# Kernel optimization log

Measured on AMD Instinct MI355X. Metric: run time of the kernel, lower is better.

Reference implementation:

```python
import jax, jax.numpy as jnp
import numpy as np

LENGTH = 200
SHIFT = 150
NFFT = 256
EPS = 1e-7  # keras backend epsilon
LN10 = float(np.log(10.0))


def _make_kernels():
    # real_kernel[n, k] = cos(2*pi*k*n/nfft); imag_kernel[n, k] = -sin(2*pi*k*n/nfft)
    # taps k >= length are zeroed in the original (kernel[length-nfft:] = 0),
    # so we build the truncated [nfft, length] kernels directly.
    n = np.arange(NFFT)[:, None]
    k = np.arange(LENGTH)[None, :]
    ang = 2.0 * np.pi * n * k / NFFT
    real = np.cos(ang).astype(np.float32)
    imag = (-np.sin(ang)).astype(np.float32)
    return jnp.asarray(real), jnp.asarray(imag)


def setup_inputs() -> dict:
    key = jax.random.key(0)
    B = 64
    S = 200 + 150 * 3199  # 480050, satisfies (S - length) % shift == 0
    x = jax.random.normal(key, (B, S, 1), dtype=jnp.float32)
    real_kernel, imag_kernel = _make_kernels()
    return {"x": x, "real_kernel": real_kernel, "imag_kernel": imag_kernel}


def reference(x, real_kernel, imag_kernel):
    B, S, C = x.shape  # C == 1
    # normalize_signal: zero mean / unit std over (time, channel)
    mu = jnp.mean(x, axis=(1, 2), keepdims=True)
    sd = jnp.std(x, axis=(1, 2), keepdims=True)
    x = (x - mu) / (sd + EPS)

    sig = x[:, :, 0]  # [B, S]
    T = (S - LENGTH) // SHIFT + 1  # frames; zero-padding to nfft is a no-op since padded taps hit zeroed kernel rows
    idx = SHIFT * jnp.arange(T)[:, None] + jnp.arange(LENGTH)[None, :]  # [T, length]
    frames = sig[:, idx]  # [B, T, length]

    # strided conv1d against dense DFT kernels == framed GEMM
    real_part = jnp.einsum("btl,nl->btn", frames, real_kernel)  # [B, T, nfft]
    imag_part = jnp.einsum("btl,nl->btn", frames, imag_kernel)

    # mode == 'log': log10 of clipped magnitude
    mag = jnp.sqrt(jnp.square(real_part) + jnp.square(imag_part))
    fft = jnp.log(jnp.maximum(mag, EPS)) / LN10

    # permute (0,2,1) -> [B, nfft, T], keep first nfft//2 bins, add channel dim
    fft = jnp.transpose(fft, (0, 2, 1))[:, : NFFT // 2, :, None]  # [B, 128, T, 1]

    # normalize_feature: zero mean / unit std over frequency axis
    fmu = jnp.mean(fft, axis=1, keepdims=True)
    fsd = jnp.std(fft, axis=1, keepdims=True)
    fft = (fft - fmu) / (fsd + EPS)
    return fft
```

## Files before the change

### kernel.cpp

```cpp
#include <hip/hip_runtime.h>
#include <math.h>
#include <stdint.h>

#define BATCH 64
#define SLEN  480050
#define TFR   3200
#define FLEN  200
#define FSH   150
#define NBINS 128
#define NCOL  256
#define NKC   7

#define WS_SUM 0
#define WS_MU  2048
#define WS_OR  2112
#define WS_OI  2240
#define WS_TABI_BYTES 16384

typedef __attribute__((ext_vector_type(8))) short bf16x8;
typedef __attribute__((ext_vector_type(4))) float f32x4;

__device__ inline unsigned pack2bf(float a, float b) {
    unsigned ua = __builtin_bit_cast(unsigned, a);
    unsigned ub = __builtin_bit_cast(unsigned, b);
    ua = (ua + 0x7FFFu + ((ua >> 16) & 1u)) >> 16;
    ub = (ub + 0x7FFFu + ((ub >> 16) & 1u)) >> 16;
    return ua | (ub << 16);
}

__device__ inline void gll16(const void* g, void* l) {
    __builtin_amdgcn_global_load_lds(
        (const __attribute__((address_space(1))) void*)g,
        (__attribute__((address_space(3))) void*)l, 16, 0, 0);
}

__global__ __launch_bounds__(256) void k_sum_partial(const float* __restrict__ x,
                                                     float* __restrict__ ws) {
    int blk = blockIdx.x;
    int b = blk >> 5, c = blk & 31;
    const float2* row = (const float2*)(x + (size_t)b * SLEN);
    const int n2 = SLEN / 2;
    const int per = (n2 + 31) / 32;
    int start = c * per;
    int end = start + per; if (end > n2) end = n2;
    float s = 0.f;
    for (int i = start + threadIdx.x; i < end; i += 256) {
        float2 v = row[i];
        s += v.x + v.y;
    }
    #pragma unroll
    for (int off = 1; off < 64; off <<= 1) s += __shfl_xor(s, off);
    __shared__ float ls[4];
    int wave = threadIdx.x >> 6, lane = threadIdx.x & 63;
    if (lane == 0) ls[wave] = s;
    __syncthreads();
    if (threadIdx.x == 0)
        ws[WS_SUM + b * 32 + c] = ls[0] + ls[1] + ls[2] + ls[3];
}

__global__ __launch_bounds__(64) void k_final(float* __restrict__ ws) {
    int b = threadIdx.x;
    if (b < BATCH) {
        float s = 0.f;
        #pragma unroll
        for (int c = 0; c < 32; ++c) s += ws[WS_SUM + b * 32 + c];
        ws[WS_MU + b] = s / (float)SLEN;
    }
}

__global__ __launch_bounds__(256) void k_colsum(const float* __restrict__ rk,
                                                const float* __restrict__ ik,
                                                float* __restrict__ ws) {
    int n = blockIdx.x;
    int l = threadIdx.x;
    float cr = 0.f, ci = 0.f;
    if (l < FLEN) {
        cr = rk[n * FLEN + l];
        ci = ik[n * FLEN + l];
    }
    #pragma unroll
    for (int off = 1; off < 64; off <<= 1) {
        cr += __shfl_xor(cr, off);
        ci += __shfl_xor(ci, off);
    }
    __shared__ float lr[4], li[4];
    int wave = threadIdx.x >> 6, lane = threadIdx.x & 63;
    if (lane == 0) { lr[wave] = cr; li[wave] = ci; }
    __syncthreads();
    if (threadIdx.x == 0) {
        ws[WS_OR + n] = lr[0] + lr[1] + lr[2] + lr[3];
        ws[WS_OI + n] = li[0] + li[1] + li[2] + li[3];
    }
}

__global__ __launch_bounds__(256) void k_tabsplit(const float* __restrict__ rk,
                                                  const float* __restrict__ ik,
                                                  float* __restrict__ ws) {
    int e = blockIdx.x * 256 + threadIdx.x;
    if (e >= NCOL * 112) return;
    int c = e / 112;
    int p = e - c * 112;
    int k = p * 2;
    int n = c & 127;
    const float* src = (c & 128) ? ik : rk;
    float v0 = (k     < FLEN) ? src[n * FLEN + k]     : 0.f;
    float v1 = (k + 1 < FLEN) ? src[n * FLEN + k + 1] : 0.f;
    unsigned hi = pack2bf(v0, v1);
    float h0 = __builtin_bit_cast(float, hi << 16);
    float h1 = __builtin_bit_cast(float, hi & 0xFFFF0000u);
    unsigned lo = pack2bf(v0 - h0, v1 - h1);
    int kc = k >> 5;
    int kb = (k & 31) * 2;
    int sb = (kb >> 4) ^ ((c >> 1) & 3);
    char* base = (char*)ws + WS_TABI_BYTES + kc * 32768 + c * 64 + (sb << 4) + (kb & 15);
    *(unsigned*)base = hi;
    *(unsigned*)(base + 16384) = lo;
}

__global__ __launch_bounds__(256, 2) void k_main(const float* __restrict__ x,
                                                 const float* __restrict__ ws,
                                                 float* __restrict__ out) {
    __shared__ __align__(16) unsigned char smem[65536];

    const int tid    = threadIdx.x;
    const int b      = blockIdx.y;
    const int t0     = blockIdx.x * 64;
    const int lane   = tid & 63;
    const int w      = tid >> 6;
    const int lanelo = lane & 15;
    const int lq     = lane >> 4;
    const int sbswz  = (lanelo >> 1) & 3;

    const float* xb  = x + (size_t)b * SLEN;
    const char* tabI = (const char*)ws + WS_TABI_BYTES;

    #pragma unroll
    for (int i = 0; i < 8; ++i)
        gll16(tabI + (w * 8 + i) * 1024 + lane * 16, smem + (w * 8 + i) * 1024);
    __syncthreads();

    f32x4 acc[16];
    #pragma unroll
    for (int nt = 0; nt < 16; ++nt) acc[nt] = (f32x4){0.f, 0.f, 0.f, 0.f};

    const float* arow = xb + (size_t)(t0 + w * 16 + lanelo) * FSH;

    for (int kc = 0; kc < NKC; ++kc) {
        if (kc < NKC - 1) {
            const char* src = tabI + (size_t)(kc + 1) * 32768;
            unsigned char* db = smem + ((kc + 1) & 1) * 32768;
            #pragma unroll
            for (int i = 0; i < 8; ++i)
                gll16(src + (w * 8 + i) * 1024 + lane * 16, db + (w * 8 + i) * 1024);
        }

        float a[8];
        if (kc < NKC - 1 || lq == 0) {
            const float2* s2 = (const float2*)(arow + kc * 32 + lq * 8);
            float2 p0 = s2[0], p1 = s2[1], p2 = s2[2], p3 = s2[3];
            a[0] = p0.x; a[1] = p0.y; a[2] = p1.x; a[3] = p1.y;
            a[4] = p2.x; a[5] = p2.y; a[6] = p3.x; a[7] = p3.y;
        } else {
            #pragma unroll
            for (int i = 0; i < 8; ++i) a[i] = 0.f;
        }
        unsigned hw[4], lw[4];
        #pragma unroll
        for (int q = 0; q < 4; ++q) {
            hw[q] = pack2bf(a[2 * q], a[2 * q + 1]);
            float h0 = __builtin_bit_cast(float, hw[q] << 16);
            float h1 = __builtin_bit_cast(float, hw[q] & 0xFFFF0000u);
            lw[q] = pack2bf(a[2 * q] - h0, a[2 * q + 1] - h1);
        }
        bf16x8 ah = __builtin_bit_cast(bf16x8, *(uint4*)hw);
        bf16x8 al = __builtin_bit_cast(bf16x8, *(uint4*)lw);

        const unsigned char* Bb = smem + (kc & 1) * 32768;
        #pragma unroll
        for (int nt = 0; nt < 16; ++nt) {
            int off = (nt * 16 + lanelo) * 64 + ((lq ^ sbswz) << 4);
            bf16x8 bh = *(const bf16x8*)(Bb + off);
            bf16x8 bl = *(const bf16x8*)(Bb + 16384 + off);
            acc[nt] = __builtin_amdgcn_mfma_f32_16x16x32_bf16(al, bh, acc[nt], 0, 0, 0);
            acc[nt] = __builtin_amdgcn_mfma_f32_16x16x32_bf16(ah, bl, acc[nt], 0, 0, 0);
            acc[nt] = __builtin_amdgcn_mfma_f32_16x16x32_bf16(ah, bh, acc[nt], 0, 0, 0);
        }
        __syncthreads();
    }

    float mu = ws[WS_MU + b];
    float v[8][4];
    #pragma unroll
    for (int nt = 0; nt < 8; ++nt) {
        float orr = ws[WS_OR + nt * 16 + lanelo];
        float oii = ws[WS_OI + nt * 16 + lanelo];
        #pragma unroll
        for (int j = 0; j < 4; ++j) {
            float re = acc[nt][j]     - mu * orr;
            float im = acc[nt + 8][j] - mu * oii;
            float s = fmaf(re, re, im * im);
            float lg = 0.5f * __log2f(s);
            v[nt][j] = fmaxf(lg, -23.2534966f);
        }
    }
    #pragma unroll
    for (int j = 0; j < 4; ++j) {
        float s = 0.f, q = 0.f;
        #pragma unroll
        for (int nt = 0; nt < 8; ++nt) {
            s += v[nt][j];
            q = fmaf(v[nt][j], v[nt][j], q);
        }
        #pragma unroll
        for (int off = 1; off < 16; off <<= 1) {
            s += __shfl_xor(s, off);
            q += __shfl_xor(q, off);
        }
        float mean = s * (1.f / 128.f);
        float var  = fmaxf(q * (1.f / 128.f) - mean * mean, 0.f);
        float sc   = 1.f / (sqrtf(var) + 3.3219281e-7f);
        #pragma unroll
        for (int nt = 0; nt < 8; ++nt) v[nt][j] = (v[nt][j] - mean) * sc;
    }

    float* Tw = (float*)(smem + w * 8192);
    #pragma unroll
    for (int nt = 0; nt < 8; ++nt) {
        int n = nt * 16 + lanelo;
        int swzl = (lq ^ (n & 3) ^ ((n >> 2) & 1)) << 2;
        *(float4*)(Tw + n * 16 + swzl) =
            make_float4(v[nt][0], v[nt][1], v[nt][2], v[nt][3]);
    }
    float* ob = out + (size_t)b * NBINS * TFR + t0 + w * 16;
    #pragma unroll
    for (int p = 0; p < 2; ++p) {
        int n = p * 64 + lane;
        int sw = (n & 3) ^ ((n >> 2) & 1);
        float4 r0 = *(float4*)(Tw + n * 16 + ((0 ^ sw) << 2));
        float4 r1 = *(float4*)(Tw + n * 16 + ((1 ^ sw) << 2));
        float4 r2 = *(float4*)(Tw + n * 16 + ((2 ^ sw) << 2));
        float4 r3 = *(float4*)(Tw + n * 16 + ((3 ^ sw) << 2));
        float4* dst = (float4*)(ob + (size_t)n * TFR);
        dst[0] = r0; dst[1] = r1; dst[2] = r2; dst[3] = r3;
    }
}

extern "C" void kernel_launch(void* const* d_in, const int* in_sizes, int n_in,
                              void* d_out, int out_size, void* d_ws, size_t ws_size,
                              hipStream_t stream) {
    const float* x  = (const float*)d_in[0];
    const float* rk = (const float*)d_in[1];
    const float* ik = (const float*)d_in[2];
    float* out = (float*)d_out;
    float* ws  = (float*)d_ws;

    k_sum_partial<<<BATCH * 32, 256, 0, stream>>>(x, ws);
    k_final<<<1, 64, 0, stream>>>(ws);
    k_colsum<<<NBINS, 256, 0, stream>>>(rk, ik, ws);
    k_tabsplit<<<112, 256, 0, stream>>>(rk, ik, ws);
    k_main<<<dim3(TFR / 64, BATCH), 256, 0, stream>>>(x, ws, out);
}
```

Measured before the change: 316.4 us.

## Merge prep kernels into one launch and double M-tile per wave in main GEMM

Folds the four preprocessing kernels into a single k_aux launch. The per-batch mean is now computed inside k_main from the partial sums, which removes launch overhead and one dependent launch. k_main now processes 128 frames per block, two 16-row M tiles per wave, so each B fragment loaded from LDS feeds six MFMAs instead of three and the table staging is amortised over twice the frames. The input split now uses the hip bf16 conversion intrinsics. Costs are twice the accumulator registers (128 floats) under a 2-blocks-per-CU bound, which risks spills, and half as many blocks (1600), which reduces parallelism.

```diff
diff --git a/kernel.cpp b/kernel.cpp
--- a/kernel.cpp
+++ b/kernel.cpp
@@ -1,4 +1,5 @@
 #include <hip/hip_runtime.h>
+#include <hip/hip_bf16.h>
 #include <math.h>
 #include <stdint.h>
 
@@ -12,7 +13,6 @@
 #define NKC   7
 
 #define WS_SUM 0
-#define WS_MU  2048
 #define WS_OR  2112
 #define WS_OI  2240
 #define WS_TABI_BYTES 16384
@@ -34,87 +34,83 @@
         (__attribute__((address_space(3))) void*)l, 16, 0, 0);
 }
 
-__global__ __launch_bounds__(256) void k_sum_partial(const float* __restrict__ x,
-                                                     float* __restrict__ ws) {
+__global__ __launch_bounds__(256) void k_aux(const float* __restrict__ x,
+                                             const float* __restrict__ rk,
+                                             const float* __restrict__ ik,
+                                             float* __restrict__ ws) {
     int blk = blockIdx.x;
-    int b = blk >> 5, c = blk & 31;
-    const float2* row = (const float2*)(x + (size_t)b * SLEN);
-    const int n2 = SLEN / 2;
-    const int per = (n2 + 31) / 32;
-    int start = c * per;
-    int end = start + per; if (end > n2) end = n2;
-    float s = 0.f;
-    for (int i = start + threadIdx.x; i < end; i += 256) {
-        float2 v = row[i];
-        s += v.x + v.y;
-    }
-    #pragma unroll
-    for (int off = 1; off < 64; off <<= 1) s += __shfl_xor(s, off);
-    __shared__ float ls[4];
-    int wave = threadIdx.x >> 6, lane = threadIdx.x & 63;
-    if (lane == 0) ls[wave] = s;
-    __syncthreads();
-    if (threadIdx.x == 0)
-        ws[WS_SUM + b * 32 + c] = ls[0] + ls[1] + ls[2] + ls[3];
-}
-
-__global__ __launch_bounds__(64) void k_final(float* __restrict__ ws) {
-    int b = threadIdx.x;
-    if (b < BATCH) {
+    if (blk < 2048) {
+        int b = blk >> 5, c = blk & 31;
+        const float2* row = (const float2*)(x + (size_t)b * SLEN);
+        const int n2 = SLEN / 2;
+        const int per = (n2 + 31) / 32;
+        int start = c * per;
+        int end = start + per; if (end > n2) end = n2;
         float s = 0.f;
-        #pragma unroll
-        for (int c = 0; c < 32; ++c) s += ws[WS_SUM + b * 32 + c];
-        ws[WS_MU + b] = s / (float)SLEN;
-    }
-}
-
-__global__ __launch_bounds__(256) void k_colsum(const float* __restrict__ rk,
-                                                const float* __restrict__ ik,
-                                                float* __restrict__ ws) {
-    int n = blockIdx.x;
-    int l = threadIdx.x;
-    float cr = 0.f, ci = 0.f;
-    if (l < FLEN) {
-        cr = rk[n * FLEN + l];
-        ci = ik[n * FLEN + l];
-    }
-    #pragma unroll
-    for (int off = 1; off < 64; off <<= 1) {
-        cr += __shfl_xor(cr, off);
-        ci += __shfl_xor(ci, off);
-    }
-    __shared__ float lr[4], li[4];
-    int wave = threadIdx.x >> 6, lane = threadIdx.x & 63;
-    if (lane == 0) { lr[wave] = cr; li[wave] = ci; }
-    __syncthreads();
-    if (threadIdx.x == 0) {
-        ws[WS_OR + n] = lr[0] + lr[1] + lr[2] + lr[3];
-        ws[WS_OI + n] = li[0] + li[1] + li[2] + li[3];
-    }
-}
-
-__global__ __launch_bounds__(256) void k_tabsplit(const float* __restrict__ rk,
-                                                  const float* __restrict__ ik,
-                                                  float* __restrict__ ws) {
-    int e = blockIdx.x * 256 + threadIdx.x;
-    if (e >= NCOL * 112) return;
-    int c = e / 112;
-    int p = e - c * 112;
-    int k = p * 2;
-    int n = c & 127;
-    const float* src = (c & 128) ? ik : rk;
-    float v0 = (k     < FLEN) ? src[n * FLEN + k]     : 0.f;
-    float v1 = (k + 1 < FLEN) ? src[n * FLEN + k + 1] : 0.f;
-    unsigned hi = pack2bf(v0, v1);
-    float h0 = __builtin_bit_cast(float, hi << 16);
-    float h1 = __builtin_bit_cast(float, hi & 0xFFFF0000u);
-    unsigned lo = pack2bf(v0 - h0, v1 - h1);
-    int kc = k >> 5;
-    int kb = (k & 31) * 2;
-    int sb = (kb >> 4) ^ ((c >> 1) & 3);
-    char* base = (char*)ws + WS_TABI_BYTES + kc * 32768 + c * 64 + (sb << 4) + (kb & 15);
-    *(unsigned*)base = hi;
-    *(unsigned*)(base + 16384) = lo;
+        for (int i = start + threadIdx.x; i < end; i += 256) {
+            float2 v = row[i];
+            s += v.x + v.y;
+        }
+        #pragma unroll
+        for (int off = 1; off < 64; off <<= 1) s += __shfl_xor(s, off);
+        __shared__ float ls[4];
+        int wave = threadIdx.x >> 6, lane = threadIdx.x & 63;
+        if (lane == 0) ls[wave] = s;
+        __syncthreads();
+        if (threadIdx.x == 0)
+            ws[WS_SUM + b * 32 + c] = ls[0] + ls[1] + ls[2] + ls[3];
+    } else if (blk < 2160) {
+        int e = (blk - 2048) * 256 + threadIdx.x;
+        int c = e / 112;
+        int p = e - c * 112;
+        int k = p * 2;
+        int n = c & 127;
+        const float* src = (c & 128) ? ik : rk;
+        float v0 = (k     < FLEN) ? src[n * FLEN + k]     : 0.f;
+        float v1 = (k + 1 < FLEN) ? src[n * FLEN + k + 1] : 0.f;
+        unsigned hi = pack2bf(v0, v1);
+        float h0 = __builtin_bit_cast(float, hi << 16);
+        float h1 = __builtin_bit_cast(float, hi & 0xFFFF0000u);
+        unsigned lo = pack2bf(v0 - h0, v1 - h1);
+        int kc = k >> 5;
+        int kb = (k & 31) * 2;
+        int sb = (kb >> 4) ^ ((c >> 1) & 3);
+        char* base = (char*)ws + WS_TABI_BYTES + kc * 32768 + c * 64 + (sb << 4) + (kb & 15);
+        *(unsigned*)base = hi;
+        *(unsigned*)(base + 16384) = lo;
+    } else {
+        int n = blk - 2160;
+        int l = threadIdx.x;
+        float cr = 0.f, ci = 0.f;
+        if (l < FLEN) {
+            cr = rk[n * FLEN + l];
+            ci = ik[n * FLEN + l];
+        }
+        #pragma unroll
+        for (int off = 1; off < 64; off <<= 1) {
+            cr += __shfl_xor(cr, off);
+            ci += __shfl_xor(ci, off);
+        }
+        __shared__ float lr[4], li[4];
+        int wave = threadIdx.x >> 6, lane = threadIdx.x & 63;
+        if (lane == 0) { lr[wave] = cr; li[wave] = ci; }
+        __syncthreads();
+        if (threadIdx.x == 0) {
+            ws[WS_OR + n] = lr[0] + lr[1] + lr[2] + lr[3];
+            ws[WS_OI + n] = li[0] + li[1] + li[2] + li[3];
+        }
+    }
+}
+
+__device__ inline void split8(const float* __restrict__ a, bf16x8& hv, bf16x8& lv) {
+    #pragma unroll
+    for (int i = 0; i < 8; ++i) {
+        __hip_bfloat16 hb = __float2bfloat16(a[i]);
+        float hf = __bfloat162float(hb);
+        __hip_bfloat16 lb = __float2bfloat16(a[i] - hf);
+        hv[i] = __builtin_bit_cast(short, hb);
+        lv[i] = __builtin_bit_cast(short, lb);
+    }
 }
 
 __global__ __launch_bounds__(256, 2) void k_main(const float* __restrict__ x,
@@ -124,7 +120,7 @@
 
     const int tid    = threadIdx.x;
     const int b      = blockIdx.y;
-    const int t0     = blockIdx.x * 64;
+    const int t0     = blockIdx.x * 128;
     const int lane   = tid & 63;
     const int w      = tid >> 6;
     const int lanelo = lane & 15;
@@ -134,16 +130,22 @@
     const float* xb  = x + (size_t)b * SLEN;
     const char* tabI = (const char*)ws + WS_TABI_BYTES;
 
+    float msum = 0.f;
+    #pragma unroll
+    for (int c = 0; c < 32; ++c) msum += ws[WS_SUM + b * 32 + c];
+    const float mu = msum * (1.0f / (float)SLEN);
+
     #pragma unroll
     for (int i = 0; i < 8; ++i)
         gll16(tabI + (w * 8 + i) * 1024 + lane * 16, smem + (w * 8 + i) * 1024);
     __syncthreads();
 
-    f32x4 acc[16];
-    #pragma unroll
-    for (int nt = 0; nt < 16; ++nt) acc[nt] = (f32x4){0.f, 0.f, 0.f, 0.f};
-
-    const float* arow = xb + (size_t)(t0 + w * 16 + lanelo) * FSH;
+    f32x4 acc[32];
+    #pragma unroll
+    for (int q = 0; q < 32; ++q) acc[q] = (f32x4){0.f, 0.f, 0.f, 0.f};
+
+    const float* arow0 = xb + (size_t)(t0 + w * 32 + lanelo) * FSH;
+    const float* arow1 = arow0 + (size_t)16 * FSH;
 
     for (int kc = 0; kc < NKC; ++kc) {
         if (kc < NKC - 1) {
@@ -154,26 +156,22 @@
                 gll16(src + (w * 8 + i) * 1024 + lane * 16, db + (w * 8 + i) * 1024);
         }
 
-        float a[8];
-        if (kc < NKC - 1 || lq == 0) {
-            const float2* s2 = (const float2*)(arow + kc * 32 + lq * 8);
-            float2 p0 = s2[0], p1 = s2[1], p2 = s2[2], p3 = s2[3];
-            a[0] = p0.x; a[1] = p0.y; a[2] = p1.x; a[3] = p1.y;
-            a[4] = p2.x; a[5] = p2.y; a[6] = p3.x; a[7] = p3.y;
-        } else {
-            #pragma unroll
-            for (int i = 0; i < 8; ++i) a[i] = 0.f;
-        }
-        unsigned hw[4], lw[4];
-        #pragma unroll
-        for (int q = 0; q < 4; ++q) {
-            hw[q] = pack2bf(a[2 * q], a[2 * q + 1]);
-            float h0 = __builtin_bit_cast(float, hw[q] << 16);
-            float h1 = __builtin_bit_cast(float, hw[q] & 0xFFFF0000u);
-            lw[q] = pack2bf(a[2 * q] - h0, a[2 * q + 1] - h1);
-        }
-        bf16x8 ah = __builtin_bit_cast(bf16x8, *(uint4*)hw);
-        bf16x8 al = __builtin_bit_cast(bf16x8, *(uint4*)lw);
+        bf16x8 ah[2], al[2];
+        #pragma unroll
+        for (int m = 0; m < 2; ++m) {
+            const float* ar = m ? arow1 : arow0;
+            float a[8];
+            if (kc < NKC - 1 || lq == 0) {
+                const float2* s2 = (const float2*)(ar + kc * 32 + lq * 8);
+                float2 p0 = s2[0], p1 = s2[1], p2 = s2[2], p3 = s2[3];
+                a[0] = p0.x; a[1] = p0.y; a[2] = p1.x; a[3] = p1.y;
+                a[4] = p2.x; a[5] = p2.y; a[6] = p3.x; a[7] = p3.y;
+            } else {
+                #pragma unroll
+                for (int i = 0; i < 8; ++i) a[i] = 0.f;
+            }
+            split8(a, ah[m], al[m]);
+        }
 
         const unsigned char* Bb = smem + (kc & 1) * 32768;
         #pragma unroll
@@ -181,67 +179,73 @@
             int off = (nt * 16 + lanelo) * 64 + ((lq ^ sbswz) << 4);
             bf16x8 bh = *(const bf16x8*)(Bb + off);
             bf16x8 bl = *(const bf16x8*)(Bb + 16384 + off);
-            acc[nt] = __builtin_amdgcn_mfma_f32_16x16x32_bf16(al, bh, acc[nt], 0, 0, 0);
-            acc[nt] = __builtin_amdgcn_mfma_f32_16x16x32_bf16(ah, bl, acc[nt], 0, 0, 0);
-            acc[nt] = __builtin_amdgcn_mfma_f32_16x16x32_bf16(ah, bh, acc[nt], 0, 0, 0);
+            #pragma unroll
+            for (int m = 0; m < 2; ++m) {
+                f32x4 t = acc[m * 16 + nt];
+                t = __builtin_amdgcn_mfma_f32_16x16x32_bf16(al[m], bh, t, 0, 0, 0);
+                t = __builtin_amdgcn_mfma_f32_16x16x32_bf16(ah[m], bl, t, 0, 0, 0);
+                t = __builtin_amdgcn_mfma_f32_16x16x32_bf16(ah[m], bh, t, 0, 0, 0);
+                acc[m * 16 + nt] = t;
+            }
         }
         __syncthreads();
     }
 
-    float mu = ws[WS_MU + b];
-    float v[8][4];
-    #pragma unroll
-    for (int nt = 0; nt < 8; ++nt) {
-        float orr = ws[WS_OR + nt * 16 + lanelo];
-        float oii = ws[WS_OI + nt * 16 + lanelo];
+    float* Tw = (float*)(smem + w * 8192);
+    #pragma unroll
+    for (int m = 0; m < 2; ++m) {
+        float v[8][4];
+        #pragma unroll
+        for (int nt = 0; nt < 8; ++nt) {
+            float orr = ws[WS_OR + nt * 16 + lanelo];
+            float oii = ws[WS_OI + nt * 16 + lanelo];
+            #pragma unroll
+            for (int j = 0; j < 4; ++j) {
+                float re = acc[m * 16 + nt][j]     - mu * orr;
+                float im = acc[m * 16 + nt + 8][j] - mu * oii;
+                float s2 = fmaf(re, re, im * im);
+                float lg = 0.5f * __log2f(s2);
+                v[nt][j] = fmaxf(lg, -23.2534966f);
+            }
+        }
         #pragma unroll
         for (int j = 0; j < 4; ++j) {
-            float re = acc[nt][j]     - mu * orr;
-            float im = acc[nt + 8][j] - mu * oii;
-            float s = fmaf(re, re, im * im);
-            float lg = 0.5f * __log2f(s);
-            v[nt][j] = fmaxf(lg, -23.2534966f);
-        }
-    }
-    #pragma unroll
-    for (int j = 0; j < 4; ++j) {
-        float s = 0.f, q = 0.f;
+            float s = 0.f, q = 0.f;
+            #pragma unroll
+            for (int nt = 0; nt < 8; ++nt) {
+                s += v[nt][j];
+                q = fmaf(v[nt][j], v[nt][j], q);
+            }
+            #pragma unroll
+            for (int off = 1; off < 16; off <<= 1) {
+                s += __shfl_xor(s, off);
+                q += __shfl_xor(q, off);
+            }
+            float mean = s * (1.f / 128.f);
+            float var  = fmaxf(q * (1.f / 128.f) - mean * mean, 0.f);
+            float sc   = 1.f / (sqrtf(var) + 3.3219281e-7f);
+            #pragma unroll
+            for (int nt = 0; nt < 8; ++nt) v[nt][j] = (v[nt][j] - mean) * sc;
+        }
         #pragma unroll
         for (int nt = 0; nt < 8; ++nt) {
-            s += v[nt][j];
-            q = fmaf(v[nt][j], v[nt][j], q);
-        }
-        #pragma unroll
-        for (int off = 1; off < 16; off <<= 1) {
-            s += __shfl_xor(s, off);
-            q += __shfl_xor(q, off);
-        }
-        float mean = s * (1.f / 128.f);
-        float var  = fmaxf(q * (1.f / 128.f) - mean * mean, 0.f);
-        float sc   = 1.f / (sqrtf(var) + 3.3219281e-7f);
-        #pragma unroll
-        for (int nt = 0; nt < 8; ++nt) v[nt][j] = (v[nt][j] - mean) * sc;
-    }
-
-    float* Tw = (float*)(smem + w * 8192);
-    #pragma unroll
-    for (int nt = 0; nt < 8; ++nt) {
-        int n = nt * 16 + lanelo;
-        int swzl = (lq ^ (n & 3) ^ ((n >> 2) & 1)) << 2;
-        *(float4*)(Tw + n * 16 + swzl) =
-            make_float4(v[nt][0], v[nt][1], v[nt][2], v[nt][3]);
-    }
-    float* ob = out + (size_t)b * NBINS * TFR + t0 + w * 16;
-    #pragma unroll
-    for (int p = 0; p < 2; ++p) {
-        int n = p * 64 + lane;
-        int sw = (n & 3) ^ ((n >> 2) & 1);
-        float4 r0 = *(float4*)(Tw + n * 16 + ((0 ^ sw) << 2));
-        float4 r1 = *(float4*)(Tw + n * 16 + ((1 ^ sw) << 2));
-        float4 r2 = *(float4*)(Tw + n * 16 + ((2 ^ sw) << 2));
-        float4 r3 = *(float4*)(Tw + n * 16 + ((3 ^ sw) << 2));
-        float4* dst = (float4*)(ob + (size_t)n * TFR);
-        dst[0] = r0; dst[1] = r1; dst[2] = r2; dst[3] = r3;
+            int n = nt * 16 + lanelo;
+            int swzl = (lq ^ (n & 3) ^ ((n >> 2) & 1)) << 2;
+            *(float4*)(Tw + n * 16 + swzl) =
+                make_float4(v[nt][0], v[nt][1], v[nt][2], v[nt][3]);
+        }
+        float* ob = out + (size_t)b * NBINS * TFR + t0 + w * 32 + m * 16;
+        #pragma unroll
+        for (int p = 0; p < 2; ++p) {
+            int n = p * 64 + lane;
+            int sw = (n & 3) ^ ((n >> 2) & 1);
+            float4 r0 = *(float4*)(Tw + n * 16 + ((0 ^ sw) << 2));
+            float4 r1 = *(float4*)(Tw + n * 16 + ((1 ^ sw) << 2));
+            float4 r2 = *(float4*)(Tw + n * 16 + ((2 ^ sw) << 2));
+            float4 r3 = *(float4*)(Tw + n * 16 + ((3 ^ sw) << 2));
+            float4* dst = (float4*)(ob + (size_t)n * TFR);
+            dst[0] = r0; dst[1] = r1; dst[2] = r2; dst[3] = r3;
+        }
     }
 }
 
@@ -254,9 +258,6 @@
     float* out = (float*)d_out;
     float* ws  = (float*)d_ws;
 
-    k_sum_partial<<<BATCH * 32, 256, 0, stream>>>(x, ws);
-    k_final<<<1, 64, 0, stream>>>(ws);
-    k_colsum<<<NBINS, 256, 0, stream>>>(rk, ik, ws);
-    k_tabsplit<<<112, 256, 0, stream>>>(rk, ik, ws);
-    k_main<<<dim3(TFR / 64, BATCH), 256, 0, stream>>>(x, ws, out);
-}
+    k_aux<<<2288, 256, 0, stream>>>(x, rk, ik, ws);
+    k_main<<<dim3(TFR / 128, BATCH), 256, 0, stream>>>(x, ws, out);
+}
```

After: 314.2 us. About the same (-0.7%).
